# Optimization experiments

Hardware: AMD Instinct MI355X
Metric: run time of the kernel (lower is better)

The kernel has to match this reference:

```python
import jax, jax.numpy as jnp
import numpy as np

H, F, E, TOPK = 2048, 8192, 8, 2
B, S = 2, 256


def setup_inputs() -> dict:
    key = jax.random.key(0)
    kx, kg, k1, k2, k3 = jax.random.split(key, 5)
    scale = 0.02
    return {
        "x": jax.random.normal(kx, (B, S, H), dtype=jnp.float32),
        "Wg": jax.random.normal(kg, (H, E), dtype=jnp.float32) * scale,
        "W1": jax.random.normal(k1, (E, H, F), dtype=jnp.float32) * scale,
        "W2": jax.random.normal(k2, (E, F, H), dtype=jnp.float32) * scale,
        "W3": jax.random.normal(k3, (E, H, F), dtype=jnp.float32) * scale,
    }


def reference(x, Wg, W1, W2, W3):
    B_, S_, H_ = x.shape
    xf = x.reshape(-1, H_)                      # [T, H]
    T = xf.shape[0]

    # Router: gate logits -> softmax -> top-k, renormalize selected weights.
    logits = xf @ Wg                            # [T, E]
    probs = jax.nn.softmax(logits, axis=-1)
    topw, topi = jax.lax.top_k(probs, TOPK)     # [T, K]
    topw = topw / jnp.sum(topw, axis=-1, keepdims=True)

    # Combine matrix: combine[t, e] = routing weight of expert e for token t (0 if unselected).
    combine = jnp.zeros((T, E), dtype=x.dtype).at[jnp.arange(T)[:, None], topi].add(topw)

    # Per-expert gated MLP (dense over experts; zeros in `combine` drop unselected experts).
    h1 = jnp.einsum("th,ehf->etf", xf, W1)      # [E, T, F]
    h3 = jnp.einsum("th,ehf->etf", xf, W3)      # [E, T, F]
    h = jax.nn.relu(h1) * h3                    # gated activation
    ye = jnp.einsum("etf,efh->eth", h, W2)      # [E, T, H]

    out = jnp.einsum("eth,te->th", ye, combine) # scatter-add combine
    return out.reshape(B_, S_, H_)
```

## Files before the change

### kernel.cpp

```cpp
#include <hip/hip_runtime.h>
#include <hip/hip_bf16.h>


#define HDIM 2048
#define FDIM 8192
#define NEXP 8
#define NTOK 512
#define MAXT 512

typedef __attribute__((ext_vector_type(8))) short short8;
typedef __attribute__((ext_vector_type(4))) float f32x4;
typedef unsigned int u32;
typedef unsigned short u16;

__device__ __forceinline__ unsigned cvtpk(float lo, float hi) {
    unsigned r;
    asm("v_cvt_pk_bf16_f32 %0, %1, %2" : "=v"(r) : "v"(lo), "v"(hi));
    return r;
}
__device__ __forceinline__ unsigned f2bf1(float f) {
    unsigned u = __builtin_bit_cast(unsigned, f);
    return (u + 0x7FFFu + ((u >> 16) & 1u)) >> 16;
}
__device__ __forceinline__ void gload16(const void* g, void* l) {
    __builtin_amdgcn_global_load_lds((const __attribute__((address_space(1))) u32*)g,
                                     (__attribute__((address_space(3))) u32*)l, 16, 0, 0);
}

#define A_OFF(r, k) (((((r)*64) + (k)) * 2) ^ ((((r) & 7)) << 4))

__global__ void moe_router(const float* __restrict__ x, const float* __restrict__ Wg,
                           int* __restrict__ counts, int* __restrict__ tok_id,
                           float* __restrict__ tok_w) {
    const int t = blockIdx.x;
    const int lane = threadIdx.x;
    const float* xr = x + (size_t)t * HDIM;
    float acc[8];
    #pragma unroll
    for (int e = 0; e < 8; ++e) acc[e] = 0.f;
    #pragma unroll 4
    for (int i = 0; i < HDIM / 64; ++i) {
        int h = lane + i * 64;
        float xv = xr[h];
        const float4* wr = (const float4*)(Wg + (size_t)h * 8);
        float4 wa = wr[0], wb = wr[1];
        acc[0] += xv * wa.x; acc[1] += xv * wa.y; acc[2] += xv * wa.z; acc[3] += xv * wa.w;
        acc[4] += xv * wb.x; acc[5] += xv * wb.y; acc[6] += xv * wb.z; acc[7] += xv * wb.w;
    }
    #pragma unroll
    for (int off = 32; off >= 1; off >>= 1) {
        #pragma unroll
        for (int e = 0; e < 8; ++e) acc[e] += __shfl_xor(acc[e], off);
    }
    if (lane == 0) {
        int e0 = 0;
        #pragma unroll
        for (int e = 1; e < 8; ++e) if (acc[e] > acc[e0]) e0 = e;
        int e1 = (e0 == 0) ? 1 : 0;
        #pragma unroll
        for (int e = 0; e < 8; ++e) if (e != e0 && acc[e] > acc[e1]) e1 = e;
        float w0 = 1.f / (1.f + __expf(acc[e1] - acc[e0]));
        float w1 = 1.f - w0;
        int s0 = atomicAdd(&counts[e0], 1);
        tok_id[e0 * MAXT + s0] = t; tok_w[e0 * MAXT + s0] = w0;
        int s1 = atomicAdd(&counts[e1], 1);
        tok_id[e1 * MAXT + s1] = t; tok_w[e1 * MAXT + s1] = w1;
    }
}

__global__ void moe_scan(const int* __restrict__ counts, int* __restrict__ offsets) {
    if (threadIdx.x == 0) {
        int a = 0;
        for (int e = 0; e < NEXP; ++e) { offsets[e] = a; a += counts[e]; }
    }
}

__global__ void moe_xcvt(const float* __restrict__ x, u16* __restrict__ xbf) {
    const int i = (blockIdx.x * 256 + threadIdx.x) * 8;
    float4 a = *(const float4*)(x + i);
    float4 b = *(const float4*)(x + i + 4);
    uint4 q;
    q.x = cvtpk(a.x, a.y); q.y = cvtpk(a.z, a.w);
    q.z = cvtpk(b.x, b.y); q.w = cvtpk(b.z, b.w);
    *(uint4*)(xbf + i) = q;
}

__device__ __forceinline__ short8 bfrag(const float* sB, int kbase, int nsw) {
    const float* p = sB + kbase * 64 + nsw;
    float f[8];
    #pragma unroll
    for (int j = 0; j < 8; ++j) f[j] = p[j * 64];
    uint4 q;
    q.x = cvtpk(f[0], f[1]); q.y = cvtpk(f[2], f[3]);
    q.z = cvtpk(f[4], f[5]); q.w = cvtpk(f[6], f[7]);
    return __builtin_bit_cast(short8, q);
}

__global__ __launch_bounds__(256, 3)
void moe_gemm1(const u16* __restrict__ xbf, const float* __restrict__ W1,
               const float* __restrict__ W3, const int* __restrict__ counts,
               const int* __restrict__ offsets, const int* __restrict__ tok_id,
               u16* __restrict__ hbuf) {
    const int nt = blockIdx.x, mt = blockIdx.y, e = blockIdx.z;
    const int cnt = counts[e];
    if (mt * 128 >= cnt) return;
    const int n0 = nt * 64;
    const int tid = threadIdx.x;
    const int w = tid >> 6, l = tid & 63;

    __shared__ __align__(16) unsigned char sA[128 * 64 * 2];
    __shared__ __align__(16) float sB1[64 * 64];
    __shared__ __align__(16) float sB3[64 * 64];

    const int ar = (l >> 3), ac = l & 7;
    const u16* asrc[4];
    #pragma unroll
    for (int p = 0; p < 4; ++p) {
        int row = w * 32 + p * 8 + ar;
        int slot = mt * 128 + row;
        int tok = tok_id[e * MAXT + (slot < cnt ? slot : cnt - 1)];
        asrc[p] = xbf + (size_t)tok * HDIM + (ac ^ (row & 7)) * 8;
    }
    const int kr = (l >> 4), c4 = l & 15;
    const size_t wstride = (size_t)HDIM * FDIM;
    size_t bsrc[4];
    #pragma unroll
    for (int p = 0; p < 4; ++p) {
        int krow = w * 16 + p * 4 + kr;
        bsrc[p] = (size_t)e * wstride + (size_t)krow * FDIM + n0 +
                  (size_t)((c4 ^ (((krow >> 3) & 1) << 2)) * 4);
    }

    const int wr = (w >> 1) * 64, wc = (w & 1) * 32;
    const int lr = l & 15, lg = l >> 4;
    const int lk = lg * 8;
    const int g1 = lg & 1;

    f32x4 acc1[4][2], acc3[4][2];
    #pragma unroll
    for (int mi = 0; mi < 4; ++mi)
        #pragma unroll
        for (int ni = 0; ni < 2; ++ni) { acc1[mi][ni] = (f32x4)0.f; acc3[mi][ni] = (f32x4)0.f; }

    for (int kt = 0; kt < HDIM / 64; ++kt) {
        #pragma unroll
        for (int p = 0; p < 4; ++p) {
            gload16(asrc[p] + kt * 64, &sA[(w * 32 + p * 8) * 128]);
            gload16(W1 + bsrc[p] + (size_t)kt * 64 * FDIM, &sB1[(w * 16 + p * 4) * 64]);
            gload16(W3 + bsrc[p] + (size_t)kt * 64 * FDIM, &sB3[(w * 16 + p * 4) * 64]);
        }
        __syncthreads();
        #pragma unroll
        for (int ks = 0; ks < 2; ++ks) {
            const int kk = ks * 32 + lk;
            short8 a[4];
            #pragma unroll
            for (int mi = 0; mi < 4; ++mi)
                a[mi] = *(const short8*)&sA[A_OFF(wr + mi * 16 + lr, kk)];
            #pragma unroll
            for (int ni = 0; ni < 2; ++ni) {
                const int nsw = (wc + ni * 16 + lr) ^ (g1 << 4);
                short8 b1 = bfrag(sB1, kk, nsw);
                short8 b3 = bfrag(sB3, kk, nsw);
                #pragma unroll
                for (int mi = 0; mi < 4; ++mi) {
                    acc1[mi][ni] = __builtin_amdgcn_mfma_f32_16x16x32_bf16(a[mi], b1, acc1[mi][ni], 0, 0, 0);
                    acc3[mi][ni] = __builtin_amdgcn_mfma_f32_16x16x32_bf16(a[mi], b3, acc3[mi][ni], 0, 0, 0);
                }
            }
        }
        __syncthreads();
    }
    const int hbase = offsets[e] + mt * 128;
    #pragma unroll
    for (int mi = 0; mi < 4; ++mi)
        #pragma unroll
        for (int ni = 0; ni < 2; ++ni)
            #pragma unroll
            for (int r = 0; r < 4; ++r) {
                int rl = wr + mi * 16 + (l >> 4) * 4 + r;
                int sl = mt * 128 + rl;
                if (sl < cnt) {
                    float v1 = acc1[mi][ni][r];
                    v1 = v1 > 0.f ? v1 : 0.f;
                    float hv = v1 * acc3[mi][ni][r];
                    hbuf[(size_t)(hbase + rl) * FDIM + (n0 + wc + ni * 16 + lr)] =
                        (u16)f2bf1(hv);
                }
            }
}

__global__ __launch_bounds__(256, 4)
void moe_gemm2(const u16* __restrict__ hbuf, const float* __restrict__ W2,
               const int* __restrict__ counts, const int* __restrict__ offsets,
               const int* __restrict__ tok_id, const float* __restrict__ tok_w,
               float* __restrict__ out) {
    const int nt = blockIdx.x, e = blockIdx.z;
    const int mt = blockIdx.y & 3, ksp = blockIdx.y >> 2;
    const int cnt = counts[e];
    if (mt * 128 >= cnt) return;
    const int n0 = nt * 64;
    const int tid = threadIdx.x;
    const int w = tid >> 6, l = tid & 63;

    __shared__ __align__(16) unsigned char sA[128 * 64 * 2];
    __shared__ __align__(16) float sB[64 * 64];

    const int ar = (l >> 3), ac = l & 7;
    const u16* asrc[4];
    #pragma unroll
    for (int p = 0; p < 4; ++p) {
        int row = w * 32 + p * 8 + ar;
        int hrow = offsets[e] + mt * 128 + row;
        asrc[p] = hbuf + (size_t)hrow * FDIM + ksp * 2048 + (ac ^ (row & 7)) * 8;
    }
    const int kr = (l >> 4), c4 = l & 15;
    size_t bsrc[4];
    #pragma unroll
    for (int p = 0; p < 4; ++p) {
        int krow = w * 16 + p * 4 + kr;
        bsrc[p] = (size_t)e * ((size_t)FDIM * HDIM) + (size_t)(ksp * 2048 + krow) * HDIM +
                  n0 + (size_t)((c4 ^ (((krow >> 3) & 1) << 2)) * 4);
    }

    const int wr = (w >> 1) * 64, wc = (w & 1) * 32;
    const int lr = l & 15, lg = l >> 4;
    const int lk = lg * 8;
    const int g1 = lg & 1;

    f32x4 acc[4][2];
    #pragma unroll
    for (int mi = 0; mi < 4; ++mi)
        #pragma unroll
        for (int ni = 0; ni < 2; ++ni) acc[mi][ni] = (f32x4)0.f;

    for (int kt = 0; kt < 32; ++kt) {
        #pragma unroll
        for (int p = 0; p < 4; ++p) {
            gload16(asrc[p] + kt * 64, &sA[(w * 32 + p * 8) * 128]);
            gload16(W2 + bsrc[p] + (size_t)kt * 64 * HDIM, &sB[(w * 16 + p * 4) * 64]);
        }
        __syncthreads();
        #pragma unroll
        for (int ks = 0; ks < 2; ++ks) {
            const int kk = ks * 32 + lk;
            short8 a[4];
            #pragma unroll
            for (int mi = 0; mi < 4; ++mi)
                a[mi] = *(const short8*)&sA[A_OFF(wr + mi * 16 + lr, kk)];
            #pragma unroll
            for (int ni = 0; ni < 2; ++ni) {
                const int nsw = (wc + ni * 16 + lr) ^ (g1 << 4);
                short8 b = bfrag(sB, kk, nsw);
                #pragma unroll
                for (int mi = 0; mi < 4; ++mi)
                    acc[mi][ni] = __builtin_amdgcn_mfma_f32_16x16x32_bf16(a[mi], b, acc[mi][ni], 0, 0, 0);
            }
        }
        __syncthreads();
    }
    #pragma unroll
    for (int mi = 0; mi < 4; ++mi)
        #pragma unroll
        for (int ni = 0; ni < 2; ++ni)
            #pragma unroll
            for (int r = 0; r < 4; ++r) {
                int rl = wr + mi * 16 + (l >> 4) * 4 + r;
                int sl = mt * 128 + rl;
                if (sl < cnt) {
                    int tk = tok_id[e * MAXT + sl];
                    float wgt = tok_w[e * MAXT + sl];
                    atomicAdd(&out[(size_t)tk * HDIM + (n0 + wc + ni * 16 + lr)],
                              wgt * acc[mi][ni][r]);
                }
            }
}

extern "C" void kernel_launch(void* const* d_in, const int* in_sizes, int n_in,
                              void* d_out, int out_size, void* d_ws, size_t ws_size,
                              hipStream_t stream) {
    const float* x  = (const float*)d_in[0];
    const float* Wg = (const float*)d_in[1];
    const float* W1 = (const float*)d_in[2];
    const float* W2 = (const float*)d_in[3];
    const float* W3 = (const float*)d_in[4];
    float* out = (float*)d_out;

    char* ws = (char*)d_ws;
    int*   counts  = (int*)(ws + 0);
    int*   offsets = (int*)(ws + 32);
    int*   tok_id  = (int*)(ws + 64);
    float* tok_w   = (float*)(ws + 64 + NEXP * MAXT * 4);
    u16*   xbf     = (u16*)(ws + 65536);
    u16*   hbuf    = (u16*)(ws + 65536 + (size_t)NTOK * HDIM * 2);

    hipMemsetAsync(ws, 0, 64, stream);
    hipMemsetAsync(d_out, 0, (size_t)out_size * sizeof(float), stream);

    moe_router<<<NTOK, 64, 0, stream>>>(x, Wg, counts, tok_id, tok_w);
    moe_scan<<<1, 64, 0, stream>>>(counts, offsets);
    moe_xcvt<<<NTOK * HDIM / (256 * 8), 256, 0, stream>>>(x, xbf);
    moe_gemm1<<<dim3(FDIM / 64, 4, NEXP), 256, 0, stream>>>(xbf, W1, W3, counts, offsets, tok_id, hbuf);
    moe_gemm2<<<dim3(HDIM / 64, 16, NEXP), 256, 0, stream>>>(hbuf, W2, counts, offsets, tok_id, tok_w, out);
}
```

Before: 481.1 us.

## Double-buffer LDS tiles in both MoE GEMMs to overlap loads with MFMA

Both expert GEMM kernels now keep two LDS stages and issue the async global-to-LDS loads for tile k+1 before computing tile k. A partial vmcnt wait lets the next tile's loads stay in flight, and raw s_barrier replaces __syncthreads. The aim is to hide global memory latency behind MFMA work. In exchange LDS use doubles and launch bounds drop (3→1, 4→2), which lowers occupancy, and correctness depends on the hand-counted vmcnt values.

```diff
diff --git a/kernel.cpp b/kernel.cpp
--- a/kernel.cpp
+++ b/kernel.cpp
@@ -96,7 +96,7 @@
     return __builtin_bit_cast(short8, q);
 }
 
-__global__ __launch_bounds__(256, 3)
+__global__ __launch_bounds__(256, 1)
 void moe_gemm1(const u16* __restrict__ xbf, const float* __restrict__ W1,
                const float* __restrict__ W3, const int* __restrict__ counts,
                const int* __restrict__ offsets, const int* __restrict__ tok_id,
@@ -108,9 +108,9 @@
     const int tid = threadIdx.x;
     const int w = tid >> 6, l = tid & 63;
 
-    __shared__ __align__(16) unsigned char sA[128 * 64 * 2];
-    __shared__ __align__(16) float sB1[64 * 64];
-    __shared__ __align__(16) float sB3[64 * 64];
+    __shared__ __align__(16) unsigned char sA[2][128 * 64 * 2];
+    __shared__ __align__(16) float sB1[2][64 * 64];
+    __shared__ __align__(16) float sB3[2][64 * 64];
 
     const int ar = (l >> 3), ac = l & 7;
     const u16* asrc[4];
@@ -142,26 +142,37 @@
         #pragma unroll
         for (int ni = 0; ni < 2; ++ni) { acc1[mi][ni] = (f32x4)0.f; acc3[mi][ni] = (f32x4)0.f; }
 
+    #define STAGE1(buf, kt)                                                              \
+        _Pragma("unroll")                                                                \
+        for (int p = 0; p < 4; ++p) {                                                    \
+            gload16(asrc[p] + (kt) * 64, &sA[buf][(w * 32 + p * 8) * 128]);              \
+            gload16(W1 + bsrc[p] + (size_t)(kt) * 64 * FDIM, &sB1[buf][(w * 16 + p * 4) * 64]); \
+            gload16(W3 + bsrc[p] + (size_t)(kt) * 64 * FDIM, &sB3[buf][(w * 16 + p * 4) * 64]); \
+        }
+
+    STAGE1(0, 0);
     for (int kt = 0; kt < HDIM / 64; ++kt) {
-        #pragma unroll
-        for (int p = 0; p < 4; ++p) {
-            gload16(asrc[p] + kt * 64, &sA[(w * 32 + p * 8) * 128]);
-            gload16(W1 + bsrc[p] + (size_t)kt * 64 * FDIM, &sB1[(w * 16 + p * 4) * 64]);
-            gload16(W3 + bsrc[p] + (size_t)kt * 64 * FDIM, &sB3[(w * 16 + p * 4) * 64]);
-        }
-        __syncthreads();
+        const int cur = kt & 1;
+        if (kt + 1 < HDIM / 64) {
+            STAGE1(cur ^ 1, kt + 1);
+            asm volatile("s_waitcnt vmcnt(12)" ::: "memory");
+        } else {
+            asm volatile("s_waitcnt vmcnt(0)" ::: "memory");
+        }
+        __builtin_amdgcn_s_barrier();
+        asm volatile("" ::: "memory");
         #pragma unroll
         for (int ks = 0; ks < 2; ++ks) {
             const int kk = ks * 32 + lk;
             short8 a[4];
             #pragma unroll
             for (int mi = 0; mi < 4; ++mi)
-                a[mi] = *(const short8*)&sA[A_OFF(wr + mi * 16 + lr, kk)];
+                a[mi] = *(const short8*)&sA[cur][A_OFF(wr + mi * 16 + lr, kk)];
             #pragma unroll
             for (int ni = 0; ni < 2; ++ni) {
                 const int nsw = (wc + ni * 16 + lr) ^ (g1 << 4);
-                short8 b1 = bfrag(sB1, kk, nsw);
-                short8 b3 = bfrag(sB3, kk, nsw);
+                short8 b1 = bfrag(sB1[cur], kk, nsw);
+                short8 b3 = bfrag(sB3[cur], kk, nsw);
                 #pragma unroll
                 for (int mi = 0; mi < 4; ++mi) {
                     acc1[mi][ni] = __builtin_amdgcn_mfma_f32_16x16x32_bf16(a[mi], b1, acc1[mi][ni], 0, 0, 0);
@@ -169,7 +180,8 @@
                 }
             }
         }
-        __syncthreads();
+        asm volatile("" ::: "memory");
+        __builtin_amdgcn_s_barrier();
     }
     const int hbase = offsets[e] + mt * 128;
     #pragma unroll
@@ -190,7 +202,7 @@
             }
 }
 
-__global__ __launch_bounds__(256, 4)
+__global__ __launch_bounds__(256, 2)
 void moe_gemm2(const u16* __restrict__ hbuf, const float* __restrict__ W2,
                const int* __restrict__ counts, const int* __restrict__ offsets,
                const int* __restrict__ tok_id, const float* __restrict__ tok_w,
@@ -203,8 +215,8 @@
     const int tid = threadIdx.x;
     const int w = tid >> 6, l = tid & 63;
 
-    __shared__ __align__(16) unsigned char sA[128 * 64 * 2];
-    __shared__ __align__(16) float sB[64 * 64];
+    __shared__ __align__(16) unsigned char sA[2][128 * 64 * 2];
+    __shared__ __align__(16) float sB[2][64 * 64];
 
     const int ar = (l >> 3), ac = l & 7;
     const u16* asrc[4];
@@ -234,30 +246,42 @@
         #pragma unroll
         for (int ni = 0; ni < 2; ++ni) acc[mi][ni] = (f32x4)0.f;
 
+    #define STAGE2(buf, kt)                                                          \
+        _Pragma("unroll")                                                            \
+        for (int p = 0; p < 4; ++p) {                                                \
+            gload16(asrc[p] + (kt) * 64, &sA[buf][(w * 32 + p * 8) * 128]);          \
+            gload16(W2 + bsrc[p] + (size_t)(kt) * 64 * HDIM, &sB[buf][(w * 16 + p * 4) * 64]); \
+        }
+
+    STAGE2(0, 0);
     for (int kt = 0; kt < 32; ++kt) {
-        #pragma unroll
-        for (int p = 0; p < 4; ++p) {
-            gload16(asrc[p] + kt * 64, &sA[(w * 32 + p * 8) * 128]);
-            gload16(W2 + bsrc[p] + (size_t)kt * 64 * HDIM, &sB[(w * 16 + p * 4) * 64]);
-        }
-        __syncthreads();
+        const int cur = kt & 1;
+        if (kt + 1 < 32) {
+            STAGE2(cur ^ 1, kt + 1);
+            asm volatile("s_waitcnt vmcnt(8)" ::: "memory");
+        } else {
+            asm volatile("s_waitcnt vmcnt(0)" ::: "memory");
+        }
+        __builtin_amdgcn_s_barrier();
+        asm volatile("" ::: "memory");
         #pragma unroll
         for (int ks = 0; ks < 2; ++ks) {
             const int kk = ks * 32 + lk;
             short8 a[4];
             #pragma unroll
             for (int mi = 0; mi < 4; ++mi)
-                a[mi] = *(const short8*)&sA[A_OFF(wr + mi * 16 + lr, kk)];
+                a[mi] = *(const short8*)&sA[cur][A_OFF(wr + mi * 16 + lr, kk)];
             #pragma unroll
             for (int ni = 0; ni < 2; ++ni) {
                 const int nsw = (wc + ni * 16 + lr) ^ (g1 << 4);
-                short8 b = bfrag(sB, kk, nsw);
+                short8 b = bfrag(sB[cur], kk, nsw);
                 #pragma unroll
                 for (int mi = 0; mi < 4; ++mi)
                     acc[mi][ni] = __builtin_amdgcn_mfma_f32_16x16x32_bf16(a[mi], b, acc[mi][ni], 0, 0, 0);
             }
         }
-        __syncthreads();
+        asm volatile("" ::: "memory");
+        __builtin_amdgcn_s_barrier();
     }
     #pragma unroll
     for (int mi = 0; mi < 4; ++mi)
```

Result: slower. 592.2 us (+23.1%).

## Double-buffer both MoE GEMMs with register-staged A tiles and K=32 steps

Applied to the files above, without the earlier changes.

Both expert GEMM kernels now use double-buffered LDS and a K-step of 32 instead of 64. The A tile is loaded through registers into a padded LDS layout, while the fp32 weight tile is prefetched directly into LDS for the next step. Manual s_waitcnt, raw s_barrier and sched_barrier calls overlap the next step's global loads with the current step's MFMAs, replacing the load-then-sync-then-compute pattern. The change doubles the number of barriers per K, and the occupancy hint drops to 2 waves per SIMD, which may leave less latency hiding than before.

```diff
diff --git a/kernel.cpp b/kernel.cpp
--- a/kernel.cpp
+++ b/kernel.cpp
@@ -26,8 +26,7 @@
     __builtin_amdgcn_global_load_lds((const __attribute__((address_space(1))) u32*)g,
                                      (__attribute__((address_space(3))) u32*)l, 16, 0, 0);
 }
-
-#define A_OFF(r, k) (((((r)*64) + (k)) * 2) ^ ((((r) & 7)) << 4))
+#define SBAR() __builtin_amdgcn_sched_barrier(0)
 
 __global__ void moe_router(const float* __restrict__ x, const float* __restrict__ Wg,
                            int* __restrict__ counts, int* __restrict__ tok_id,
@@ -96,7 +95,7 @@
     return __builtin_bit_cast(short8, q);
 }
 
-__global__ __launch_bounds__(256, 3)
+__global__ __launch_bounds__(256, 2)
 void moe_gemm1(const u16* __restrict__ xbf, const float* __restrict__ W1,
                const float* __restrict__ W3, const int* __restrict__ counts,
                const int* __restrict__ offsets, const int* __restrict__ tok_id,
@@ -108,27 +107,25 @@
     const int tid = threadIdx.x;
     const int w = tid >> 6, l = tid & 63;
 
-    __shared__ __align__(16) unsigned char sA[128 * 64 * 2];
-    __shared__ __align__(16) float sB1[64 * 64];
-    __shared__ __align__(16) float sB3[64 * 64];
-
-    const int ar = (l >> 3), ac = l & 7;
-    const u16* asrc[4];
-    #pragma unroll
-    for (int p = 0; p < 4; ++p) {
-        int row = w * 32 + p * 8 + ar;
-        int slot = mt * 128 + row;
-        int tok = tok_id[e * MAXT + (slot < cnt ? slot : cnt - 1)];
-        asrc[p] = xbf + (size_t)tok * HDIM + (ac ^ (row & 7)) * 8;
-    }
-    const int kr = (l >> 4), c4 = l & 15;
+    __shared__ __align__(16) u16 sApad[2][128 * 40];
+    __shared__ __align__(16) float sB1[2][2048];
+    __shared__ __align__(16) float sB3[2][2048];
+
+    const int arow = tid >> 1;
+    const int akc = (tid & 1) * 16;
+    const int aslot = mt * 128 + arow;
+    const int atok = tok_id[e * MAXT + (aslot < cnt ? aslot : cnt - 1)];
+    const u16* areg_src = xbf + (size_t)atok * HDIM + akc;
+
+    const int kr = l >> 4, c4 = l & 15;
     const size_t wstride = (size_t)HDIM * FDIM;
-    size_t bsrc[4];
-    #pragma unroll
-    for (int p = 0; p < 4; ++p) {
-        int krow = w * 16 + p * 4 + kr;
-        bsrc[p] = (size_t)e * wstride + (size_t)krow * FDIM + n0 +
-                  (size_t)((c4 ^ (((krow >> 3) & 1) << 2)) * 4);
+    const float* b1p[2]; const float* b3p[2];
+    #pragma unroll
+    for (int i = 0; i < 2; ++i) {
+        int krow = i * 16 + w * 4 + kr;
+        size_t off = (size_t)e * wstride + (size_t)krow * FDIM + n0 +
+                     (size_t)((c4 ^ (((krow >> 3) & 1) << 2)) * 4);
+        b1p[i] = W1 + off; b3p[i] = W3 + off;
     }
 
     const int wr = (w >> 1) * 64, wc = (w & 1) * 32;
@@ -142,34 +139,58 @@
         #pragma unroll
         for (int ni = 0; ni < 2; ++ni) { acc1[mi][ni] = (f32x4)0.f; acc3[mi][ni] = (f32x4)0.f; }
 
-    for (int kt = 0; kt < HDIM / 64; ++kt) {
-        #pragma unroll
-        for (int p = 0; p < 4; ++p) {
-            gload16(asrc[p] + kt * 64, &sA[(w * 32 + p * 8) * 128]);
-            gload16(W1 + bsrc[p] + (size_t)kt * 64 * FDIM, &sB1[(w * 16 + p * 4) * 64]);
-            gload16(W3 + bsrc[p] + (size_t)kt * 64 * FDIM, &sB3[(w * 16 + p * 4) * 64]);
-        }
-        __syncthreads();
-        #pragma unroll
-        for (int ks = 0; ks < 2; ++ks) {
-            const int kk = ks * 32 + lk;
-            short8 a[4];
+    uint4 a0, a1;
+    #define ALOAD1(kt) { const u16* s_ = areg_src + (kt) * 32;                 \
+                         a0 = *(const uint4*)s_; a1 = *(const uint4*)(s_ + 8); }
+    #define AWRITE1(buf) { *(uint4*)&sApad[buf][arow * 40 + akc] = a0;         \
+                           *(uint4*)&sApad[buf][arow * 40 + akc + 8] = a1; }
+    #define BSTAGE1(buf, kt)                                                   \
+        _Pragma("unroll")                                                      \
+        for (int i = 0; i < 2; ++i) {                                          \
+            gload16(b1p[i] + (size_t)(kt) * 32 * FDIM, &sB1[buf][(i * 16 + w * 4) * 64]); \
+            gload16(b3p[i] + (size_t)(kt) * 32 * FDIM, &sB3[buf][(i * 16 + w * 4) * 64]); \
+        }
+
+    ALOAD1(0);
+    SBAR();
+    BSTAGE1(0, 0);
+    SBAR();
+    for (int kt = 0; kt < HDIM / 32; ++kt) {
+        const int cur = kt & 1;
+        asm volatile("s_waitcnt vmcnt(4)" ::: "memory");
+        SBAR();
+        AWRITE1(cur);
+        SBAR();
+        if (kt + 1 < HDIM / 32) {
+            ALOAD1(kt + 1);
+            SBAR();
+            BSTAGE1(cur ^ 1, kt + 1);
+            SBAR();
+            asm volatile("s_waitcnt vmcnt(6) lgkmcnt(0)" ::: "memory");
+        } else {
+            asm volatile("s_waitcnt vmcnt(0) lgkmcnt(0)" ::: "memory");
+        }
+        SBAR();
+        __builtin_amdgcn_s_barrier();
+        SBAR();
+        short8 a[4];
+        #pragma unroll
+        for (int mi = 0; mi < 4; ++mi)
+            a[mi] = *(const short8*)&sApad[cur][(wr + mi * 16 + lr) * 40 + lk];
+        #pragma unroll
+        for (int ni = 0; ni < 2; ++ni) {
+            const int nsw = (wc + ni * 16 + lr) ^ (g1 << 4);
+            short8 b1 = bfrag(sB1[cur], lk, nsw);
+            short8 b3 = bfrag(sB3[cur], lk, nsw);
             #pragma unroll
-            for (int mi = 0; mi < 4; ++mi)
-                a[mi] = *(const short8*)&sA[A_OFF(wr + mi * 16 + lr, kk)];
-            #pragma unroll
-            for (int ni = 0; ni < 2; ++ni) {
-                const int nsw = (wc + ni * 16 + lr) ^ (g1 << 4);
-                short8 b1 = bfrag(sB1, kk, nsw);
-                short8 b3 = bfrag(sB3, kk, nsw);
-                #pragma unroll
-                for (int mi = 0; mi < 4; ++mi) {
-                    acc1[mi][ni] = __builtin_amdgcn_mfma_f32_16x16x32_bf16(a[mi], b1, acc1[mi][ni], 0, 0, 0);
-                    acc3[mi][ni] = __builtin_amdgcn_mfma_f32_16x16x32_bf16(a[mi], b3, acc3[mi][ni], 0, 0, 0);
-                }
+            for (int mi = 0; mi < 4; ++mi) {
+                acc1[mi][ni] = __builtin_amdgcn_mfma_f32_16x16x32_bf16(a[mi], b1, acc1[mi][ni], 0, 0, 0);
+                acc3[mi][ni] = __builtin_amdgcn_mfma_f32_16x16x32_bf16(a[mi], b3, acc3[mi][ni], 0, 0, 0);
             }
         }
-        __syncthreads();
+        SBAR();
+        __builtin_amdgcn_s_barrier();
+        SBAR();
     }
     const int hbase = offsets[e] + mt * 128;
     #pragma unroll
@@ -190,7 +211,7 @@
             }
 }
 
-__global__ __launch_bounds__(256, 4)
+__global__ __launch_bounds__(256, 2)
 void moe_gemm2(const u16* __restrict__ hbuf, const float* __restrict__ W2,
                const int* __restrict__ counts, const int* __restrict__ offsets,
                const int* __restrict__ tok_id, const float* __restrict__ tok_w,
@@ -203,24 +224,21 @@
     const int tid = threadIdx.x;
     const int w = tid >> 6, l = tid & 63;
 
-    __shared__ __align__(16) unsigned char sA[128 * 64 * 2];
-    __shared__ __align__(16) float sB[64 * 64];
-
-    const int ar = (l >> 3), ac = l & 7;
-    const u16* asrc[4];
-    #pragma unroll
-    for (int p = 0; p < 4; ++p) {
-        int row = w * 32 + p * 8 + ar;
-        int hrow = offsets[e] + mt * 128 + row;
-        asrc[p] = hbuf + (size_t)hrow * FDIM + ksp * 2048 + (ac ^ (row & 7)) * 8;
-    }
-    const int kr = (l >> 4), c4 = l & 15;
-    size_t bsrc[4];
-    #pragma unroll
-    for (int p = 0; p < 4; ++p) {
-        int krow = w * 16 + p * 4 + kr;
-        bsrc[p] = (size_t)e * ((size_t)FDIM * HDIM) + (size_t)(ksp * 2048 + krow) * HDIM +
-                  n0 + (size_t)((c4 ^ (((krow >> 3) & 1) << 2)) * 4);
+    __shared__ __align__(16) u16 sApad[2][128 * 40];
+    __shared__ __align__(16) float sB[2][2048];
+
+    const int arow = tid >> 1;
+    const int akc = (tid & 1) * 16;
+    const int hrow = offsets[e] + mt * 128 + arow;
+    const u16* areg_src = hbuf + (size_t)hrow * FDIM + ksp * 2048 + akc;
+
+    const int kr = l >> 4, c4 = l & 15;
+    const float* b2p[2];
+    #pragma unroll
+    for (int i = 0; i < 2; ++i) {
+        int krow = i * 16 + w * 4 + kr;
+        b2p[i] = W2 + (size_t)e * ((size_t)FDIM * HDIM) + (size_t)(ksp * 2048 + krow) * HDIM +
+                 n0 + (size_t)((c4 ^ (((krow >> 3) & 1) << 2)) * 4);
     }
 
     const int wr = (w >> 1) * 64, wc = (w & 1) * 32;
@@ -234,30 +252,53 @@
         #pragma unroll
         for (int ni = 0; ni < 2; ++ni) acc[mi][ni] = (f32x4)0.f;
 
-    for (int kt = 0; kt < 32; ++kt) {
-        #pragma unroll
-        for (int p = 0; p < 4; ++p) {
-            gload16(asrc[p] + kt * 64, &sA[(w * 32 + p * 8) * 128]);
-            gload16(W2 + bsrc[p] + (size_t)kt * 64 * HDIM, &sB[(w * 16 + p * 4) * 64]);
-        }
-        __syncthreads();
-        #pragma unroll
-        for (int ks = 0; ks < 2; ++ks) {
-            const int kk = ks * 32 + lk;
-            short8 a[4];
+    uint4 a0, a1;
+    #define ALOAD2(kt) { const u16* s_ = areg_src + (kt) * 32;                 \
+                         a0 = *(const uint4*)s_; a1 = *(const uint4*)(s_ + 8); }
+    #define AWRITE2(buf) { *(uint4*)&sApad[buf][arow * 40 + akc] = a0;         \
+                           *(uint4*)&sApad[buf][arow * 40 + akc + 8] = a1; }
+    #define BSTAGE2(buf, kt)                                                   \
+        _Pragma("unroll")                                                      \
+        for (int i = 0; i < 2; ++i)                                            \
+            gload16(b2p[i] + (size_t)(kt) * 32 * HDIM, &sB[buf][(i * 16 + w * 4) * 64]);
+
+    ALOAD2(0);
+    SBAR();
+    BSTAGE2(0, 0);
+    SBAR();
+    for (int kt = 0; kt < 64; ++kt) {
+        const int cur = kt & 1;
+        asm volatile("s_waitcnt vmcnt(2)" ::: "memory");
+        SBAR();
+        AWRITE2(cur);
+        SBAR();
+        if (kt + 1 < 64) {
+            ALOAD2(kt + 1);
+            SBAR();
+            BSTAGE2(cur ^ 1, kt + 1);
+            SBAR();
+            asm volatile("s_waitcnt vmcnt(4) lgkmcnt(0)" ::: "memory");
+        } else {
+            asm volatile("s_waitcnt vmcnt(0) lgkmcnt(0)" ::: "memory");
+        }
+        SBAR();
+        __builtin_amdgcn_s_barrier();
+        SBAR();
+        short8 a[4];
+        #pragma unroll
+        for (int mi = 0; mi < 4; ++mi)
+            a[mi] = *(const short8*)&sApad[cur][(wr + mi * 16 + lr) * 40 + lk];
+        #pragma unroll
+        for (int ni = 0; ni < 2; ++ni) {
+            const int nsw = (wc + ni * 16 + lr) ^ (g1 << 4);
+            short8 b = bfrag(sB[cur], lk, nsw);
             #pragma unroll
             for (int mi = 0; mi < 4; ++mi)
-                a[mi] = *(const short8*)&sA[A_OFF(wr + mi * 16 + lr, kk)];
-            #pragma unroll
-            for (int ni = 0; ni < 2; ++ni) {
-                const int nsw = (wc + ni * 16 + lr) ^ (g1 << 4);
-                short8 b = bfrag(sB, kk, nsw);
-                #pragma unroll
-                for (int mi = 0; mi < 4; ++mi)
-                    acc[mi][ni] = __builtin_amdgcn_mfma_f32_16x16x32_bf16(a[mi], b, acc[mi][ni], 0, 0, 0);
-            }
-        }
-        __syncthreads();
+                acc[mi][ni] = __builtin_amdgcn_mfma_f32_16x16x32_bf16(a[mi], b, acc[mi][ni], 0, 0, 0);
+        }
+        SBAR();
+        __builtin_amdgcn_s_barrier();
+        SBAR();
     }
     #pragma unroll
     for (int mi = 0; mi < 4; ++mi)
```

New measurement: 523.1 us. 8.7% more time.
